# Performance work log

Hardware: AMD Instinct MI355X
Metric: run time of the kernel (lower is better)

Reference implementation:

```python
import jax, jax.numpy as jnp
import numpy as np
from math import factorial, pi

LMAX = 6      # max angular momentum
NMAX = 5      # max radial index
RC = 3.0      # PolyCut cutoff radius
UNIT = RC / 3.0

_one = np.ones((LMAX + 1, LMAX + 1), np.float32)
YR = jnp.asarray(2.0 * np.tril(_one) - np.eye(LMAX + 1, dtype=np.float32))
YI = jnp.asarray(2.0 * np.triu(_one, k=1))


def _nlm(l, m):
    return float(np.sqrt((2 * l + 1) / (4 * pi) * factorial(l - m) / factorial(l + m)))


def ylm_mat(v):
    """Solid harmonics r^l Y_lm for one point v=(x,y,z).
    Layout (as in AutoForce sph_repr): Re Y_l^m at [l, l-m]; Im Y_l^m at [l-m, l] for m>0,
    so YR (2*tril-eye) weights real parts (m=0 on the diagonal, weight 1) and
    YI (2*triu(1)) weights imaginary parts, reproducing the m-sum of the power spectrum."""
    x, y, z = v[0], v[1], v[2]
    r2 = x * x + y * y + z * z
    # (x + i y)^m by recursion
    A = [jnp.ones((), v.dtype)]
    B = [jnp.zeros((), v.dtype)]
    for m in range(1, LMAX + 1):
        A.append(x * A[m - 1] - y * B[m - 1])
        B.append(x * B[m - 1] + y * A[m - 1])
    # Pi_l^m(z, r^2): homogeneous associated-Legendre part of degree l-m
    Pi = {(0, 0): jnp.ones((), v.dtype)}
    for m in range(1, LMAX + 1):
        Pi[(m, m)] = (2 * m - 1) * Pi[(m - 1, m - 1)]  # (2m-1)!!
    for m in range(0, LMAX):
        Pi[(m + 1, m)] = (2 * m + 1) * z * Pi[(m, m)]
        for l in range(m + 2, LMAX + 1):
            Pi[(l, m)] = ((2 * l - 1) * z * Pi[(l - 1, m)]
                          - (l + m - 1) * r2 * Pi[(l - 2, m)]) / (l - m)
    Y = jnp.zeros((LMAX + 1, LMAX + 1), v.dtype)
    for l in range(LMAX + 1):
        for m in range(l + 1):
            cnl = _nlm(l, m)
            Y = Y.at[l, l - m].set(cnl * Pi[(l, m)] * A[m])
            if m > 0:
                Y = Y.at[l - m, l].set(cnl * Pi[(l, m)] * B[m])
    return Y


def radial(dist):
    # PolyCut: (1 - d/rc)^2 inside rc, and its derivative
    step = (dist < RC).astype(dist.dtype)
    t = 1.0 - dist / RC
    return step * t * t, -2.0 * step * t / RC


def setup_inputs() -> dict:
    key = jax.random.key(0)
    coo = jax.random.normal(key, (150000, 3), dtype=jnp.float32)
    return {"coo": coo}


def reference(coo):
    xyz = coo / UNIT                                   # (N, 3)
    d = jnp.sqrt(jnp.sum(xyz * xyz, axis=-1))          # (N,)
    n = 2.0 * jnp.arange(NMAX + 1, dtype=coo.dtype)    # even powers 0,2,...,2*nmax
    r, dr = radial(UNIT * d)
    dr = UNIT * dr
    f = r[None] * d[None] ** n[:, None]                # (nmax+1, N)
    Y = jnp.transpose(jax.vmap(ylm_mat)(xyz), (1, 2, 0))                   # (L+1, L+1, N)
    dY = jnp.transpose(jax.vmap(jax.jacfwd(ylm_mat))(xyz), (1, 2, 0, 3))   # (L+1, L+1, N, 3)
    c = jnp.einsum('nj,lmj->nlm', f, Y)                # (nmax+1, L+1, L+1)
    # p[i,k,l] = sum_m YR[l,m]*c[i,l,m]*c[k,l,m] + sum_m YI[m,l]*c[i,m,l]*c[k,m,l]
    p = (jnp.einsum('ilm,klm,lm->ikl', c, c, YR)
         + jnp.einsum('iml,kml,ml->ikl', c, c, YI))    # (nmax+1, nmax+1, L+1)
    # hand-derived gradient chain, as in the torch module
    df = dr[None] * d[None] ** n[:, None] + r[None] * n[:, None] * d[None] ** (n[:, None] - 1.0)
    dfv = df[..., None] * xyz / d[:, None]             # (nmax+1, N, 3)
    dc = (dfv[:, None, None] * Y[None, ..., None]
          + f[:, None, None, :, None] * dY[None])      # (nmax+1, L+1, L+1, N, 3)
    # dp without materializing dnnp: contract dc with (c*YR) / (c*YI) directly
    cYr = c * YR
    cYi = c * YI
    dp = (jnp.einsum('klm,ilmjx->ikljx', cYr, dc)
          + jnp.einsum('ilm,klmjx->ikljx', cYr, dc)
          + jnp.einsum('kml,imljx->ikljx', cYi, dc)
          + jnp.einsum('iml,kmljx->ikljx', cYi, dc))   # (nmax+1, nmax+1, L+1, N, 3)
    return p, dp / UNIT
```

## Files before the change

### kernel.cpp

```cpp
#include <hip/hip_runtime.h>


#define LMAXV 6
#define NSZ 6
#define RCV 3.0f

typedef float float4v __attribute__((ext_vector_type(4)));

__device__ __forceinline__ void barrier_lds() {
    asm volatile("s_waitcnt lgkmcnt(0)" ::: "memory");
    __builtin_amdgcn_sched_barrier(0);
    __builtin_amdgcn_s_barrier();
}

constexpr double csqrt_(double x) {
    double y = x > 1.0 ? x : 1.0;
    for (int i = 0; i < 100; ++i) y = 0.5 * (y + x / y);
    return y;
}
constexpr double factd_(int n) { double r = 1.0; for (int i = 2; i <= n; ++i) r *= i; return r; }
constexpr double PI_D = 3.14159265358979323846;
struct CnlT { float v[7][7]; };
constexpr CnlT make_cnl_() {
    CnlT t{};
    for (int l = 0; l <= 6; ++l)
        for (int m = 0; m <= 6; ++m)
            t.v[l][m] = (m <= l)
                ? (float)csqrt_((2.0 * l + 1.0) / (4.0 * PI_D) * factd_(l - m) / factd_(l + m))
                : 0.0f;
    return t;
}
__device__ constexpr CnlT CNL = make_cnl_();
__device__ constexpr float DFACT[7] = {1.f, 1.f, 3.f, 15.f, 105.f, 945.f, 10395.f};
struct IctT { float v[7][7]; };
constexpr IctT make_ict_() {
    IctT t{};
    for (int l = 0; l <= 6; ++l)
        for (int m = 0; m <= 6; ++m)
            t.v[l][m] = (l > m) ? (float)(1.0 / (double)(l - m)) : 1.0f;
    return t;
}
__device__ constexpr IctT ICT = make_ict_();

__global__ void k_zero(float* __restrict__ cws) {
    int t = blockIdx.x * blockDim.x + threadIdx.x;
    if (t < NSZ * 49) cws[t] = 0.0f;
}

__global__ __launch_bounds__(256) void k_creduce(const float* __restrict__ coo,
                                                 float* __restrict__ cws, int N) {
    const int i_rad = blockIdx.y;
    float acc[7][7];
#pragma unroll
    for (int a = 0; a < 7; ++a)
#pragma unroll
        for (int b = 0; b < 7; ++b) acc[a][b] = 0.0f;

    const int stride = gridDim.x * blockDim.x;
    for (int j = blockIdx.x * blockDim.x + threadIdx.x; j < N; j += stride) {
        float x = coo[3 * j + 0], y = coo[3 * j + 1], z = coo[3 * j + 2];
        float r2 = x * x + y * y + z * z;
        float dn = sqrtf(r2);
        float tt = 1.0f - dn * (1.0f / RCV);
        float r  = (dn < RCV) ? tt * tt : 0.0f;
        float fi = r;
        for (int q = 0; q < i_rad; ++q) fi *= r2;

        float Av[7], Bv[7];
        Av[0] = 1.0f; Bv[0] = 0.0f;
#pragma unroll
        for (int m = 1; m <= 6; ++m) {
            Av[m] = x * Av[m - 1] - y * Bv[m - 1];
            Bv[m] = x * Bv[m - 1] + y * Av[m - 1];
        }

        float P1[7], P2[7];
#pragma unroll
        for (int l = 0; l <= 6; ++l) {
            float PC[7];
#pragma unroll
            for (int mm = 0; mm <= l; ++mm) {
                float pv;
                if (mm == l)            pv = DFACT[l];
                else if (mm == l - 1)   pv = (float)(2 * l - 1) * z * P1[mm];
                else {
                    float a = (float)(2 * l - 1), b = (float)(l + mm - 1);
                    pv = (a * z * P1[mm] - b * r2 * P2[mm]) * (1.0f / (float)(l - mm));
                }
                PC[mm] = pv;
                float base = fi * CNL.v[l][mm] * pv;
                acc[l][l - mm] += base * Av[mm];
                if (mm >= 1) acc[l - mm][l] += base * Bv[mm];
            }
#pragma unroll
            for (int mm = 0; mm <= l; ++mm) { P2[mm] = P1[mm]; P1[mm] = PC[mm]; }
        }
    }

    __shared__ float sblk[49];
    if (threadIdx.x < 49) sblk[threadIdx.x] = 0.0f;
    __syncthreads();
    const int lane = threadIdx.x & 63;
#pragma unroll
    for (int a = 0; a < 7; ++a)
#pragma unroll
        for (int b = 0; b < 7; ++b) {
            float v = acc[a][b];
            v += __shfl_down(v, 32);
            v += __shfl_down(v, 16);
            v += __shfl_down(v, 8);
            v += __shfl_down(v, 4);
            v += __shfl_down(v, 2);
            v += __shfl_down(v, 1);
            if (lane == 0) atomicAdd(&sblk[a * 7 + b], v);
        }
    __syncthreads();
    if (threadIdx.x < 49) atomicAdd(&cws[i_rad * 49 + threadIdx.x], sblk[threadIdx.x]);
}

__global__ void k_p(const float* __restrict__ cws, float* __restrict__ out) {
    int t = threadIdx.x;
    if (t >= 252) return;
    int i = t / 42, k = (t / 7) % 6, l = t % 7;
    const float* ci = cws + i * 49;
    const float* ck = cws + k * 49;
    float s = 0.0f;
    for (int mm = 0; mm <= l; ++mm) {
        float w = (mm == 0) ? 1.0f : 2.0f;
        s += w * ci[l * 7 + (l - mm)] * ck[l * 7 + (l - mm)];
        if (mm >= 1) s += 2.0f * ci[(l - mm) * 7 + l] * ck[(l - mm) * 7 + l];
    }
    out[t] = s;
}

__global__ __launch_bounds__(256) void k_dp(const float* __restrict__ coo,
                                            const float* __restrict__ cws,
                                            float* __restrict__ out, int N,
                                            int nblk) {
    __shared__ float sRe[7][7][6];
    __shared__ float sIm[7][7][6];
    __shared__ float stage[12][768];

    for (int s = threadIdx.x; s < 294; s += blockDim.x) {
        int k = s % 6; int lm = s / 6; int l = lm / 7; int mm = lm % 7;
        float re = 0.0f, im = 0.0f;
        if (mm <= l)            re = ((mm == 0) ? 1.0f : 2.0f) * cws[k * 49 + l * 7 + (l - mm)];
        if (mm >= 1 && mm <= l) im = 2.0f * cws[k * 49 + (l - mm) * 7 + l];
        sRe[l][mm][k] = re;
        sIm[l][mm][k] = im;
    }
    __syncthreads();

    int chunk;
    {
        const int b = blockIdx.x;
        const int q = nblk >> 3, rr = nblk & 7;
        const int xcd = b & 7, idx = b >> 3;
        chunk = (xcd < rr ? xcd * (q + 1) : rr * (q + 1) + (xcd - rr) * q) + idx;
    }
    const int j0 = chunk * 256;
    const int jj = min(j0 + (int)threadIdx.x, N - 1);

    const float x = coo[3 * jj + 0], y = coo[3 * jj + 1], z = coo[3 * jj + 2];
    const float r2 = x * x + y * y + z * z;
    const float dn = sqrtf(r2);
    const float invd = 1.0f / dn;
    const float tt = 1.0f - dn * (1.0f / RCV);
    const bool  ins = dn < RCV;
    const float r  = ins ? tt * tt : 0.0f;
    const float dr = ins ? (-2.0f / RCV) * tt : 0.0f;

    float f[NSZ], dfx[NSZ], dfy[NSZ], dfz[NSZ];
    {
        const float ux = x * invd, uy = y * invd, uz = z * invd;
        float p2 = 1.0f;
#pragma unroll
        for (int i = 0; i < NSZ; ++i) {
            f[i] = r * p2;
            float dfi = p2 * (dr + (float)(2 * i) * r * invd);
            dfx[i] = dfi * ux; dfy[i] = dfi * uy; dfz[i] = dfi * uz;
            p2 *= r2;
        }
    }

    float Av[7], Ax[7], Ay[7], Bv[7], Bx[7], By[7];
    Av[0] = 1.0f; Ax[0] = 0.0f; Ay[0] = 0.0f;
    Bv[0] = 0.0f; Bx[0] = 0.0f; By[0] = 0.0f;
#pragma unroll
    for (int m = 1; m <= 6; ++m) {
        Av[m] = x * Av[m - 1] - y * Bv[m - 1];
        Ax[m] = Av[m - 1] + x * Ax[m - 1] - y * Bx[m - 1];
        Ay[m] = -Bv[m - 1] + x * Ay[m - 1] - y * By[m - 1];
        Bv[m] = x * Bv[m - 1] + y * Av[m - 1];
        Bx[m] = Bv[m - 1] + x * Bx[m - 1] + y * Ax[m - 1];
        By[m] = Av[m - 1] + x * By[m - 1] + y * Ay[m - 1];
    }

    float P1v[7], P1z[7], P1r[7], P2v[7], P2z[7], P2r[7];
#pragma unroll
    for (int mm = 0; mm < 7; ++mm) {
        P1v[mm] = 0.f; P1z[mm] = 0.f; P1r[mm] = 0.f;
        P2v[mm] = 0.f; P2z[mm] = 0.f; P2r[mm] = 0.f;
    }

    const uint32_t sliceB = (uint32_t)N * 12u;
    const uint32_t j0b    = (uint32_t)j0 * 12u;
    const uint32_t remB   = (uint32_t)(min(256, N - j0)) * 12u;
    char* const outB = (char*)out;
    const int tid3 = (int)threadIdx.x * 3;

#pragma unroll 1
    for (int l = 0; l <= LMAXV; ++l) {
        float S[NSZ], Tx[NSZ], Ty[NSZ], Tz[NSZ];
#pragma unroll
        for (int k = 0; k < NSZ; ++k) { S[k] = 0.0f; Tx[k] = 0.0f; Ty[k] = 0.0f; Tz[k] = 0.0f; }

        const float lf  = (float)l;
        const float a2l = 2.0f * lf - 1.0f;
        const float dfl = DFACT[l];

#pragma unroll
        for (int mm = 0; mm <= 6; ++mm) {
            if (mm <= l) {
                const float b  = lf + (float)(mm - 1);
                const float ic = ICT.v[l][mm];
                float pv = (a2l * z * P1v[mm] - b * r2 * P2v[mm]) * ic;
                float pz = (a2l * (P1v[mm] + z * P1z[mm]) - b * r2 * P2z[mm]) * ic;
                float pr = (a2l * z * P1r[mm] - b * (P2v[mm] + r2 * P2r[mm])) * ic;
                if (mm == l) pv = dfl;
                P2v[mm] = P1v[mm]; P2z[mm] = P1z[mm]; P2r[mm] = P1r[mm];
                P1v[mm] = pv; P1z[mm] = pz; P1r[mm] = pr;

                const float c0  = CNL.v[l][mm];
                const float cp  = c0 * pv;
                const float prx = c0 * 2.0f * pr;
                const float gz  = c0 * pz + prx * z;

                const float ReV = cp * Av[mm];
                const float ReX = prx * x * Av[mm] + cp * Ax[mm];
                const float ReG = prx * y * Av[mm] + cp * Ay[mm];
                const float ReZ = gz * Av[mm];
#pragma unroll
                for (int k = 0; k < NSZ; ++k) {
                    const float cc = sRe[l][mm][k];
                    S[k]  += cc * ReV;
                    Tx[k] += cc * ReX;
                    Ty[k] += cc * ReG;
                    Tz[k] += cc * ReZ;
                }
                if (mm >= 1) {
                    const float ImV = cp * Bv[mm];
                    const float ImX = prx * x * Bv[mm] + cp * Bx[mm];
                    const float ImG = prx * y * Bv[mm] + cp * By[mm];
                    const float ImZ = gz * Bv[mm];
#pragma unroll
                    for (int k = 0; k < NSZ; ++k) {
                        const float cc = sIm[l][mm][k];
                        S[k]  += cc * ImV;
                        Tx[k] += cc * ImX;
                        Ty[k] += cc * ImG;
                        Tz[k] += cc * ImZ;
                    }
                }
            }
        }

        const uint32_t lbase = 1008u + (uint32_t)l * sliceB + j0b;
        const uint32_t ikstride = 7u * sliceB;
#pragma unroll
        for (int g = 0; g < 3; ++g) {
#pragma unroll
            for (int sl = 0; sl < 12; ++sl) {
                const int s = g * 12 + sl;
                const int i = s / 6, k = s % 6;
                const int a = (i < k) ? i : k;
                const int c = (i < k) ? k : i;
                const float ox = dfx[a] * S[c] + f[a] * Tx[c] + dfx[c] * S[a] + f[c] * Tx[a];
                const float oy = dfy[a] * S[c] + f[a] * Ty[c] + dfy[c] * S[a] + f[c] * Ty[a];
                const float oz = dfz[a] * S[c] + f[a] * Tz[c] + dfz[c] * S[a] + f[c] * Tz[a];
                stage[sl][tid3 + 0] = ox;
                stage[sl][tid3 + 1] = oy;
                stage[sl][tid3 + 2] = oz;
            }
            barrier_lds();
#pragma unroll
            for (int it = 0; it < 9; ++it) {
                const int slot = it * 256 + (int)threadIdx.x;
                const int sl   = slot / 192;
                const int pos  = slot - sl * 192;
                const uint32_t boff = (uint32_t)pos << 4;
                if (boff < remB) {
                    const int s = g * 12 + sl;
                    float4v v = *(const float4v*)&stage[sl][pos << 2];
                    *(float4v*)(outB + lbase + (uint32_t)s * ikstride + boff) = v;
                }
            }
            barrier_lds();
        }
    }
}

extern "C" void kernel_launch(void* const* d_in, const int* in_sizes, int n_in,
                              void* d_out, int out_size, void* d_ws, size_t ws_size,
                              hipStream_t stream) {
    const float* coo = (const float*)d_in[0];
    float* out = (float*)d_out;
    float* cws = (float*)d_ws;
    const int N = in_sizes[0] / 3;

    hipLaunchKernelGGL(k_zero, dim3(1), dim3(320), 0, stream, cws);
    hipLaunchKernelGGL(k_creduce, dim3(128, 6), dim3(256), 0, stream, coo, cws, N);
    hipLaunchKernelGGL(k_p, dim3(1), dim3(256), 0, stream, cws, out);
    const int nb = (N + 255) / 256;
    hipLaunchKernelGGL(k_dp, dim3(nb), dim3(256), 0, stream, coo, cws, out, N, nb);
}
```

Measured before the change: 144.9 us.

## Derive harmonic gradients analytically to cut register state and raise occupancy

After: 273.9 us. 1.89x slower.

```diff
diff --git a/kernel.cpp b/kernel.cpp
--- a/kernel.cpp
+++ b/kernel.cpp
@@ -133,10 +133,10 @@
     out[t] = s;
 }
 
-__global__ __launch_bounds__(256) void k_dp(const float* __restrict__ coo,
-                                            const float* __restrict__ cws,
-                                            float* __restrict__ out, int N,
-                                            int nblk) {
+__global__ __launch_bounds__(256, 4) void k_dp(const float* __restrict__ coo,
+                                               const float* __restrict__ cws,
+                                               float* __restrict__ out, int N,
+                                               int nblk) {
     __shared__ float sRe[7][7][6];
     __shared__ float sIm[7][7][6];
     __shared__ float stage[12][768];
@@ -165,42 +165,36 @@
     const float r2 = x * x + y * y + z * z;
     const float dn = sqrtf(r2);
     const float invd = 1.0f / dn;
+    const float inv2r2 = 0.5f / r2;
     const float tt = 1.0f - dn * (1.0f / RCV);
     const bool  ins = dn < RCV;
     const float r  = ins ? tt * tt : 0.0f;
     const float dr = ins ? (-2.0f / RCV) * tt : 0.0f;
-
-    float f[NSZ], dfx[NSZ], dfy[NSZ], dfz[NSZ];
+    const float ux = x * invd, uy = y * invd, uz = z * invd;
+
+    float f[NSZ], dfi[NSZ];
     {
-        const float ux = x * invd, uy = y * invd, uz = z * invd;
         float p2 = 1.0f;
 #pragma unroll
         for (int i = 0; i < NSZ; ++i) {
             f[i] = r * p2;
-            float dfi = p2 * (dr + (float)(2 * i) * r * invd);
-            dfx[i] = dfi * ux; dfy[i] = dfi * uy; dfz[i] = dfi * uz;
+            dfi[i] = p2 * (dr + (float)(2 * i) * r * invd);
             p2 *= r2;
         }
     }
 
-    float Av[7], Ax[7], Ay[7], Bv[7], Bx[7], By[7];
-    Av[0] = 1.0f; Ax[0] = 0.0f; Ay[0] = 0.0f;
-    Bv[0] = 0.0f; Bx[0] = 0.0f; By[0] = 0.0f;
+    float Av[7], Bv[7];
+    Av[0] = 1.0f; Bv[0] = 0.0f;
 #pragma unroll
     for (int m = 1; m <= 6; ++m) {
         Av[m] = x * Av[m - 1] - y * Bv[m - 1];
-        Ax[m] = Av[m - 1] + x * Ax[m - 1] - y * Bx[m - 1];
-        Ay[m] = -Bv[m - 1] + x * Ay[m - 1] - y * By[m - 1];
         Bv[m] = x * Bv[m - 1] + y * Av[m - 1];
-        Bx[m] = Bv[m - 1] + x * Bx[m - 1] + y * Ax[m - 1];
-        By[m] = Av[m - 1] + x * By[m - 1] + y * Ay[m - 1];
-    }
-
-    float P1v[7], P1z[7], P1r[7], P2v[7], P2z[7], P2r[7];
+    }
+
+    float P1v[7], P1z[7], P2v[7], P2z[7];
 #pragma unroll
     for (int mm = 0; mm < 7; ++mm) {
-        P1v[mm] = 0.f; P1z[mm] = 0.f; P1r[mm] = 0.f;
-        P2v[mm] = 0.f; P2z[mm] = 0.f; P2r[mm] = 0.f;
+        P1v[mm] = 0.f; P1z[mm] = 0.f; P2v[mm] = 0.f; P2z[mm] = 0.f;
     }
 
     const uint32_t sliceB = (uint32_t)N * 12u;
@@ -226,19 +220,21 @@
                 const float ic = ICT.v[l][mm];
                 float pv = (a2l * z * P1v[mm] - b * r2 * P2v[mm]) * ic;
                 float pz = (a2l * (P1v[mm] + z * P1z[mm]) - b * r2 * P2z[mm]) * ic;
-                float pr = (a2l * z * P1r[mm] - b * (P2v[mm] + r2 * P2r[mm])) * ic;
                 if (mm == l) pv = dfl;
-                P2v[mm] = P1v[mm]; P2z[mm] = P1z[mm]; P2r[mm] = P1r[mm];
-                P1v[mm] = pv; P1z[mm] = pz; P1r[mm] = pr;
+                const float pr = ((lf - (float)mm) * pv - z * pz) * inv2r2;
+                P2v[mm] = P1v[mm]; P2z[mm] = P1z[mm];
+                P1v[mm] = pv; P1z[mm] = pz;
 
                 const float c0  = CNL.v[l][mm];
                 const float cp  = c0 * pv;
                 const float prx = c0 * 2.0f * pr;
                 const float gz  = c0 * pz + prx * z;
+                const float pmv = cp * (float)mm;
+                const int  mp  = (mm > 0) ? mm - 1 : 0;
 
                 const float ReV = cp * Av[mm];
-                const float ReX = prx * x * Av[mm] + cp * Ax[mm];
-                const float ReG = prx * y * Av[mm] + cp * Ay[mm];
+                const float ReX = prx * x * Av[mm] + pmv * Av[mp];
+                const float ReG = prx * y * Av[mm] - pmv * Bv[mp];
                 const float ReZ = gz * Av[mm];
 #pragma unroll
                 for (int k = 0; k < NSZ; ++k) {
@@ -250,8 +246,8 @@
                 }
                 if (mm >= 1) {
                     const float ImV = cp * Bv[mm];
-                    const float ImX = prx * x * Bv[mm] + cp * Bx[mm];
-                    const float ImG = prx * y * Bv[mm] + cp * By[mm];
+                    const float ImX = prx * x * Bv[mm] + pmv * Bv[mp];
+                    const float ImG = prx * y * Bv[mm] + pmv * Av[mp];
                     const float ImZ = gz * Bv[mm];
 #pragma unroll
                     for (int k = 0; k < NSZ; ++k) {
@@ -275,9 +271,10 @@
                 const int i = s / 6, k = s % 6;
                 const int a = (i < k) ? i : k;
                 const int c = (i < k) ? k : i;
-                const float ox = dfx[a] * S[c] + f[a] * Tx[c] + dfx[c] * S[a] + f[c] * Tx[a];
-                const float oy = dfy[a] * S[c] + f[a] * Ty[c] + dfy[c] * S[a] + f[c] * Ty[a];
-                const float oz = dfz[a] * S[c] + f[a] * Tz[c] + dfz[c] * S[a] + f[c] * Tz[a];
+                const float gg = dfi[a] * S[c] + dfi[c] * S[a];
+                const float ox = ux * gg + f[a] * Tx[c] + f[c] * Tx[a];
+                const float oy = uy * gg + f[a] * Ty[c] + f[c] * Ty[a];
+                const float oz = uz * gg + f[a] * Tz[c] + f[c] * Tz[a];
                 stage[sl][tid3 + 0] = ox;
                 stage[sl][tid3 + 1] = oy;
                 stage[sl][tid3 + 2] = oz;
```
